# Kernel tuning notes

Hardware: AMD Instinct MI355X
Metric: run time of the kernel (lower is better)

Reference implementation:

```python
import jax, jax.numpy as jnp
import numpy as np

N_NODES = 2048
N_PAIRS = 65536
D = 512
P = 16


def setup_inputs() -> dict:
    key = jax.random.key(0)
    ks = jax.random.split(key, 9)
    scale = 1.0 / np.sqrt(D)
    obj_feats = jax.random.normal(ks[0], (N_NODES, D), dtype=jnp.float32)
    union_feats = jax.random.normal(ks[1], (N_PAIRS, D), dtype=jnp.float32)
    pair_idxs = jax.random.randint(ks[2], (N_PAIRS, 2), 0, N_NODES, dtype=jnp.int64)
    ws_w = jax.random.uniform(ks[3], (D, D), jnp.float32, -scale, scale)
    ws_b = jax.random.uniform(ks[4], (D,), jnp.float32, -scale, scale)
    wo_w = jax.random.uniform(ks[5], (D, D), jnp.float32, -scale, scale)
    wo_b = jax.random.uniform(ks[6], (D,), jnp.float32, -scale, scale)
    w_w = jax.random.uniform(ks[7], (P, D), jnp.float32, -scale, scale)
    w_b = jax.random.uniform(ks[8], (P,), jnp.float32, -scale, scale)
    return {
        'obj_feats': obj_feats, 'union_feats': union_feats, 'pair_idxs': pair_idxs,
        'ws_w': ws_w, 'ws_b': ws_b, 'wo_w': wo_w, 'wo_b': wo_b, 'w_w': w_w, 'w_b': w_b,
    }


def reference(obj_feats, union_feats, pair_idxs, ws_w, ws_b, wo_w, wo_b, w_w, w_b):
    n = obj_feats.shape[0]
    p = w_w.shape[0]
    # node projections: [N, D]
    s = obj_feats @ ws_w.T + ws_b
    o = obj_feats @ wo_w.T + wo_b
    # gather pair features and fuse elementwise product: [E, D]
    prod = s[pair_idxs[:, 0]] * o[pair_idxs[:, 1]] * union_feats
    # project to p attention logits per pair: [E, p]
    atten_f = prod @ w_w.T + w_b
    # scatter into dense [N, N, p]
    atten = jnp.zeros((n, n, p), dtype=obj_feats.dtype)
    atten = atten.at[pair_idxs[:, 0], pair_idxs[:, 1]].add(atten_f)
    # mask diagonal with -1e4 and softmax over axis=1 (incoming nodes)
    atten = atten - jnp.eye(n, dtype=obj_feats.dtype)[:, :, None] * 10000.0
    return jax.nn.softmax(atten, axis=1)
```

## Files before the change

kernel.cpp:

```cpp
#include <hip/hip_runtime.h>
#include <hip/hip_bf16.h>

#define N_NODES 2048
#define N_PAIRS 65536
#define DIM 512
#define NP 16
#define SLOTS 96
#define SP 520

typedef __attribute__((ext_vector_type(8))) short s16x8;
typedef __attribute__((ext_vector_type(8))) unsigned short u16x8;
typedef __attribute__((ext_vector_type(4))) float f32x4;

static __device__ __forceinline__ unsigned short f2bf(float x) {
    union { float f; unsigned int u; } v; v.f = x;
    unsigned int r = v.u + 0x7FFFu + ((v.u >> 16) & 1u);
    return (unsigned short)(r >> 16);
}
static __device__ __forceinline__ float bf2f(unsigned short u) {
    union { unsigned int u; float f; } v; v.u = ((unsigned int)u) << 16;
    return v.f;
}
static __device__ __forceinline__ u16x8 pack8(float4 a, float4 b) {
    u16x8 r;
    r[0]=f2bf(a.x); r[1]=f2bf(a.y); r[2]=f2bf(a.z); r[3]=f2bf(a.w);
    r[4]=f2bf(b.x); r[5]=f2bf(b.y); r[6]=f2bf(b.z); r[7]=f2bf(b.w);
    return r;
}
static __device__ __forceinline__ void store_nt4(float* p, float a, float b, float c, float d) {
    f32x4 v = {a, b, c, d};
    __builtin_nontemporal_store(v, (f32x4*)p);
}

#define GBM 64
#define GBN 64
#define GBK 32
#define GSA 40

__global__ __launch_bounds__(256) void gemm_so(
    const float* __restrict__ A, const float* __restrict__ Ws, const float* __restrict__ bsv,
    const float* __restrict__ Wo, const float* __restrict__ bov,
    unsigned short* __restrict__ Sb, unsigned short* __restrict__ Ob,
    int* __restrict__ rowcnt)
{
    __shared__ unsigned short As[GBM*GSA];
    __shared__ unsigned short Bs[GBN*GSA];
    const int tid = threadIdx.x;
    {
        const int bid = blockIdx.y * gridDim.x + blockIdx.x;
        if (bid < 8) rowcnt[bid*256 + tid] = 0;
    }
    const int m0 = blockIdx.y*GBM, n0 = blockIdx.x*GBN;
    const int ar = tid>>2, ac = (tid&3)*8;
    const float* Arow = A + (size_t)(m0+ar)*DIM + ac;
    const int nrow = n0 + ar;
    const float* Wrow = (nrow < DIM ? Ws + (size_t)nrow*DIM : Wo + (size_t)(nrow-DIM)*DIM) + ac;
    float4 a_r[2], b_r[2];
    a_r[0] = *(const float4*)(Arow);   a_r[1] = *(const float4*)(Arow+4);
    b_r[0] = *(const float4*)(Wrow);   b_r[1] = *(const float4*)(Wrow+4);

    const int lane = tid&63, wid = tid>>6;
    const int wm = (wid>>1)*32, wn = (wid&1)*32;
    const int fr = lane&15, ks8 = (lane>>4)*8;
    f32x4 acc[2][2] = {};
    for (int k0=0; k0<DIM; k0+=GBK) {
        *(u16x8*)&As[ar*GSA+ac] = pack8(a_r[0],a_r[1]);
        *(u16x8*)&Bs[ar*GSA+ac] = pack8(b_r[0],b_r[1]);
        __syncthreads();
        if (k0+GBK < DIM) {
            a_r[0] = *(const float4*)(Arow + k0+GBK);   a_r[1] = *(const float4*)(Arow + k0+GBK + 4);
            b_r[0] = *(const float4*)(Wrow + k0+GBK);   b_r[1] = *(const float4*)(Wrow + k0+GBK + 4);
        }
        s16x8 af[2], bfr[2];
        #pragma unroll
        for (int mi=0;mi<2;++mi) af[mi]  = *(const s16x8*)&As[(wm+mi*16+fr)*GSA + ks8];
        #pragma unroll
        for (int ni=0;ni<2;++ni) bfr[ni] = *(const s16x8*)&Bs[(wn+ni*16+fr)*GSA + ks8];
        #pragma unroll
        for (int mi=0;mi<2;++mi)
            #pragma unroll
            for (int ni=0;ni<2;++ni)
                acc[mi][ni] = __builtin_amdgcn_mfma_f32_16x16x32_bf16(af[mi], bfr[ni], acc[mi][ni], 0,0,0);
        __syncthreads();
    }
    const int rg = lane>>4;
    #pragma unroll
    for (int ni=0;ni<2;++ni) {
        const int n = n0 + wn + ni*16 + fr;
        const float bias = (n < DIM) ? bsv[n] : bov[n-DIM];
        unsigned short* dst = (n < DIM) ? (Sb + n) : (Ob + (n - DIM));
        #pragma unroll
        for (int mi=0;mi<2;++mi) {
            #pragma unroll
            for (int q=0;q<4;++q) {
                const int m = m0 + wm + mi*16 + rg*4 + q;
                dst[(size_t)m*DIM] = f2bf(acc[mi][ni][q] + bias);
            }
        }
    }
}

__global__ __launch_bounds__(256) void pairproj_k(
    const unsigned short* __restrict__ Sb, const unsigned short* __restrict__ Ob,
    const float* __restrict__ U, const int* __restrict__ idx,
    const float* __restrict__ w_w, const float* __restrict__ w_b,
    int* __restrict__ rowcnt, int* __restrict__ rowj, float* __restrict__ rowv)
{
    __shared__ unsigned short P[4*16*SP];
    const int tid = threadIdx.x;
    const int lane = tid&63, wid = tid>>6;
    const int fr = lane&15, ks8 = (lane>>4)*8;
    s16x8 wreg[16];
    #pragma unroll
    for (int st=0;st<16;++st) {
        const float4* wp = (const float4*)(w_w + (size_t)fr*DIM + st*32 + ks8);
        u16x8 t = pack8(wp[0], wp[1]);
        wreg[st] = *(s16x8*)&t;
    }
    const float wbv = w_b[fr];
    unsigned short* Pw = &P[wid*16*SP];
    const int eb = blockIdx.x*128 + wid*32;
    for (int it=0; it<2; ++it) {
        const int e0 = eb + it*16;
        #pragma unroll 4
        for (int s8=0; s8<16; ++s8) {
            const int e = e0 + s8;
            const int i = idx[2*e], j = idx[2*e+1];
            u16x8 sv = *(const u16x8*)(Sb + (size_t)i*DIM + lane*8);
            u16x8 ov = *(const u16x8*)(Ob + (size_t)j*DIM + lane*8);
            const float4* up = (const float4*)(U + (size_t)e*DIM + lane*8);
            float4 u0 = up[0], u1 = up[1];
            float4 p0, p1;
            p0.x = bf2f(sv[0])*bf2f(ov[0])*u0.x;
            p0.y = bf2f(sv[1])*bf2f(ov[1])*u0.y;
            p0.z = bf2f(sv[2])*bf2f(ov[2])*u0.z;
            p0.w = bf2f(sv[3])*bf2f(ov[3])*u0.w;
            p1.x = bf2f(sv[4])*bf2f(ov[4])*u1.x;
            p1.y = bf2f(sv[5])*bf2f(ov[5])*u1.y;
            p1.z = bf2f(sv[6])*bf2f(ov[6])*u1.z;
            p1.w = bf2f(sv[7])*bf2f(ov[7])*u1.w;
            *(u16x8*)&Pw[s8*SP + lane*8] = pack8(p0, p1);
        }
        f32x4 acc = {0.f,0.f,0.f,0.f};
        #pragma unroll
        for (int st=0;st<16;++st) {
            s16x8 af = *(const s16x8*)&Pw[fr*SP + st*32 + ks8];
            acc = __builtin_amdgcn_mfma_f32_16x16x32_bf16(af, wreg[st], acc, 0,0,0);
        }
        int iv = 0, posv = 0;
        if (lane < 16) {
            const int e = e0 + lane;
            iv = idx[2*e];
            const int jv = idx[2*e + 1];
            posv = atomicAdd(&rowcnt[iv], 1);
            if (posv < SLOTS) rowj[iv*SLOTS + posv] = jv;
        }
        const int rg = lane>>4;
        #pragma unroll
        for (int q=0;q<4;++q) {
            const int pr = rg*4 + q;
            const int ip = __shfl(iv, pr, 64);
            const int pp = __shfl(posv, pr, 64);
            if (pp < SLOTS)
                rowv[((size_t)ip*SLOTS + pp)*NP + fr] = acc[q] + wbv;
        }
    }
}

__global__ __launch_bounds__(256) void softmax_k(
    const int* __restrict__ rowcnt, const int* __restrict__ rowj,
    const float* __restrict__ rowv, float* __restrict__ out)
{
    __shared__ __align__(16) float vals[SLOTS][NP];
    __shared__ int jcol[SLOTS];
    __shared__ unsigned char dead[SLOTS];
    __shared__ float red[16][17];
    __shared__ float mP[NP], invZ[NP], bg[NP];
    __shared__ int ndistinct;
    const int i = blockIdx.x;
    const int t = threadIdx.x;
    int c = rowcnt[i];
    if (c > SLOTS) c = SLOTS;

    if (t == 0) ndistinct = 0;
    for (int a = t; a < c; a += 256) {
        jcol[a] = rowj[i*SLOTS + a];
        dead[a] = 0;
        const float4* src = (const float4*)(rowv + ((size_t)i*SLOTS + a)*NP);
        float4* dst = (float4*)vals[a];
        dst[0] = src[0]; dst[1] = src[1]; dst[2] = src[2]; dst[3] = src[3];
    }
    __syncthreads();

    for (int a = t; a < c; a += 256) {
        int j = jcol[a];
        int first = a;
        for (int b = 0; b < a; ++b) if (jcol[b] == j) { first = b; break; }
        if (first != a) {
            dead[a] = 1;
            #pragma unroll
            for (int p = 0; p < NP; ++p) atomicAdd(&vals[first][p], vals[a][p]);
        }
    }
    __syncthreads();
    for (int a = t; a < c; a += 256)
        if (!dead[a] && jcol[a] != i) atomicAdd(&ndistinct, 1);
    __syncthreads();

    const int p = t & 15, ch = t >> 4;
    float pm = 0.f;
    for (int a = ch; a < c; a += 16)
        if (!dead[a] && jcol[a] != i) pm = fmaxf(pm, vals[a][p]);
    red[ch][p] = pm;
    __syncthreads();
    if (t < NP) {
        float m = 0.f;
        #pragma unroll
        for (int k = 0; k < 16; ++k) m = fmaxf(m, red[k][t]);
        mP[t] = m;
    }
    __syncthreads();
    {
        const float m = mP[p];
        float ps = 0.f;
        for (int a = ch; a < c; a += 16)
            if (!dead[a] && jcol[a] != i) ps += __expf(vals[a][p] - m);
        red[ch][p] = ps;
    }
    __syncthreads();
    if (t < NP) {
        float zs = 0.f;
        #pragma unroll
        for (int k = 0; k < 16; ++k) zs += red[k][t];
        const float m = mP[t];
        const float eb = __expf(-m);
        const float nbg = (float)(N_NODES - 1 - ndistinct);
        const float Z = zs + nbg * eb;
        const float iz = 1.0f / Z;
        invZ[t] = iz; bg[t] = eb * iz;
    }
    __syncthreads();

    const size_t rowbase = (size_t)i * N_NODES * NP;
    {
        const int g = t & 3;
        const float b0 = bg[g*4+0], b1 = bg[g*4+1], b2 = bg[g*4+2], b3 = bg[g*4+3];
        float* orow = out + rowbase;
        #pragma unroll 8
        for (int n = 0; n < 32; ++n)
            store_nt4(orow + 4*(t + 256*n), b0, b1, b2, b3);
    }
    __syncthreads();

    for (int a = t; a < c; a += 256) {
        if (dead[a]) continue;
        const int j = jcol[a];
        float* dst = out + rowbase + (size_t)j * NP;
        if (j == i) {
            store_nt4(dst+0,  0.f,0.f,0.f,0.f);
            store_nt4(dst+4,  0.f,0.f,0.f,0.f);
            store_nt4(dst+8,  0.f,0.f,0.f,0.f);
            store_nt4(dst+12, 0.f,0.f,0.f,0.f);
        } else {
            #pragma unroll
            for (int q = 0; q < 4; ++q) {
                store_nt4(dst + 4*q,
                    __expf(vals[a][4*q+0] - mP[4*q+0]) * invZ[4*q+0],
                    __expf(vals[a][4*q+1] - mP[4*q+1]) * invZ[4*q+1],
                    __expf(vals[a][4*q+2] - mP[4*q+2]) * invZ[4*q+2],
                    __expf(vals[a][4*q+3] - mP[4*q+3]) * invZ[4*q+3]);
            }
        }
    }
    if (t == 0) {
        float* dst = out + rowbase + (size_t)i * NP;
        store_nt4(dst+0,  0.f,0.f,0.f,0.f);
        store_nt4(dst+4,  0.f,0.f,0.f,0.f);
        store_nt4(dst+8,  0.f,0.f,0.f,0.f);
        store_nt4(dst+12, 0.f,0.f,0.f,0.f);
    }
}

extern "C" void kernel_launch(void* const* d_in, const int* in_sizes, int n_in,
                              void* d_out, int out_size, void* d_ws, size_t ws_size,
                              hipStream_t stream)
{
    (void)in_sizes; (void)n_in; (void)out_size; (void)ws_size;
    const float* obj  = (const float*)d_in[0];
    const float* uni  = (const float*)d_in[1];
    const int*   idx  = (const int*)  d_in[2];
    const float* ws_w = (const float*)d_in[3];
    const float* ws_b = (const float*)d_in[4];
    const float* wo_w = (const float*)d_in[5];
    const float* wo_b = (const float*)d_in[6];
    const float* w_w  = (const float*)d_in[7];
    const float* w_b  = (const float*)d_in[8];
    float* out = (float*)d_out;

    unsigned short* Sb = (unsigned short*)d_ws;
    unsigned short* Ob = Sb + (size_t)N_NODES * DIM;
    float* rowv  = (float*)(Ob + (size_t)N_NODES * DIM);
    int* rowj    = (int*)(rowv + (size_t)N_NODES * SLOTS * NP);
    int* rowcnt  = rowj + (size_t)N_NODES * SLOTS;

    gemm_so<<<dim3(1024/GBN, N_NODES/GBM), 256, 0, stream>>>(obj, ws_w, ws_b, wo_w, wo_b, Sb, Ob, rowcnt);
    pairproj_k<<<N_PAIRS/128, 256, 0, stream>>>(Sb, Ob, uni, idx, w_w, w_b, rowcnt, rowj, rowv);
    softmax_k<<<N_NODES, 256, 0, stream>>>(rowcnt, rowj, rowv, out);
}
```

Measured before the change: 122.8 us.

## Split pair projection K dimension in halves and shrink per-block pair count

The pair projection kernel now handles 16 pairs per wave instead of 32, so the grid doubles to N_PAIRS/64 blocks. It walks the 512-wide feature dimension in two halves of 256, staging a half-width bf16 tile in shared memory and accumulating MFMA results across the halves. This halves shared memory per block and doubles the number of blocks, aiming for better occupancy and latency hiding on the gather-heavy loads. In exchange, each lane issues narrower 8-byte loads, and the 16 pre-packed weight registers are still loaded once per block, now amortised over half as many pairs.

```diff
diff --git a/kernel.cpp b/kernel.cpp
--- a/kernel.cpp
+++ b/kernel.cpp
@@ -6,10 +6,11 @@
 #define DIM 512
 #define NP 16
 #define SLOTS 96
-#define SP 520
+#define SP2 264
 
 typedef __attribute__((ext_vector_type(8))) short s16x8;
 typedef __attribute__((ext_vector_type(8))) unsigned short u16x8;
+typedef __attribute__((ext_vector_type(4))) unsigned short u16x4;
 typedef __attribute__((ext_vector_type(4))) float f32x4;
 
 static __device__ __forceinline__ unsigned short f2bf(float x) {
@@ -106,7 +107,7 @@
     const float* __restrict__ w_w, const float* __restrict__ w_b,
     int* __restrict__ rowcnt, int* __restrict__ rowj, float* __restrict__ rowv)
 {
-    __shared__ unsigned short P[4*16*SP];
+    __shared__ unsigned short P[4*16*SP2];
     const int tid = threadIdx.x;
     const int lane = tid&63, wid = tid>>6;
     const int fr = lane&15, ks8 = (lane>>4)*8;
@@ -118,52 +119,49 @@
         wreg[st] = *(s16x8*)&t;
     }
     const float wbv = w_b[fr];
-    unsigned short* Pw = &P[wid*16*SP];
-    const int eb = blockIdx.x*128 + wid*32;
-    for (int it=0; it<2; ++it) {
-        const int e0 = eb + it*16;
+    unsigned short* Pw = &P[wid*16*SP2];
+    const int e0 = blockIdx.x*64 + wid*16;
+
+    f32x4 acc = {0.f,0.f,0.f,0.f};
+    #pragma unroll
+    for (int kh=0; kh<2; ++kh) {
+        const int kb = kh*256;
         #pragma unroll 4
         for (int s8=0; s8<16; ++s8) {
             const int e = e0 + s8;
             const int i = idx[2*e], j = idx[2*e+1];
-            u16x8 sv = *(const u16x8*)(Sb + (size_t)i*DIM + lane*8);
-            u16x8 ov = *(const u16x8*)(Ob + (size_t)j*DIM + lane*8);
-            const float4* up = (const float4*)(U + (size_t)e*DIM + lane*8);
-            float4 u0 = up[0], u1 = up[1];
-            float4 p0, p1;
-            p0.x = bf2f(sv[0])*bf2f(ov[0])*u0.x;
-            p0.y = bf2f(sv[1])*bf2f(ov[1])*u0.y;
-            p0.z = bf2f(sv[2])*bf2f(ov[2])*u0.z;
-            p0.w = bf2f(sv[3])*bf2f(ov[3])*u0.w;
-            p1.x = bf2f(sv[4])*bf2f(ov[4])*u1.x;
-            p1.y = bf2f(sv[5])*bf2f(ov[5])*u1.y;
-            p1.z = bf2f(sv[6])*bf2f(ov[6])*u1.z;
-            p1.w = bf2f(sv[7])*bf2f(ov[7])*u1.w;
-            *(u16x8*)&Pw[s8*SP + lane*8] = pack8(p0, p1);
-        }
-        f32x4 acc = {0.f,0.f,0.f,0.f};
-        #pragma unroll
-        for (int st=0;st<16;++st) {
-            s16x8 af = *(const s16x8*)&Pw[fr*SP + st*32 + ks8];
-            acc = __builtin_amdgcn_mfma_f32_16x16x32_bf16(af, wreg[st], acc, 0,0,0);
-        }
-        int iv = 0, posv = 0;
-        if (lane < 16) {
-            const int e = e0 + lane;
-            iv = idx[2*e];
-            const int jv = idx[2*e + 1];
-            posv = atomicAdd(&rowcnt[iv], 1);
-            if (posv < SLOTS) rowj[iv*SLOTS + posv] = jv;
-        }
-        const int rg = lane>>4;
-        #pragma unroll
-        for (int q=0;q<4;++q) {
-            const int pr = rg*4 + q;
-            const int ip = __shfl(iv, pr, 64);
-            const int pp = __shfl(posv, pr, 64);
-            if (pp < SLOTS)
-                rowv[((size_t)ip*SLOTS + pp)*NP + fr] = acc[q] + wbv;
-        }
+            u16x4 sv = *(const u16x4*)(Sb + (size_t)i*DIM + kb + lane*4);
+            u16x4 ov = *(const u16x4*)(Ob + (size_t)j*DIM + kb + lane*4);
+            float4 uv = *(const float4*)(U + (size_t)e*DIM + kb + lane*4);
+            u16x4 pk;
+            pk[0] = f2bf(bf2f(sv[0])*bf2f(ov[0])*uv.x);
+            pk[1] = f2bf(bf2f(sv[1])*bf2f(ov[1])*uv.y);
+            pk[2] = f2bf(bf2f(sv[2])*bf2f(ov[2])*uv.z);
+            pk[3] = f2bf(bf2f(sv[3])*bf2f(ov[3])*uv.w);
+            *(u16x4*)&Pw[s8*SP2 + lane*4] = pk;
+        }
+        #pragma unroll
+        for (int st=0;st<8;++st) {
+            s16x8 af = *(const s16x8*)&Pw[fr*SP2 + st*32 + ks8];
+            acc = __builtin_amdgcn_mfma_f32_16x16x32_bf16(af, wreg[kh*8+st], acc, 0,0,0);
+        }
+    }
+    int iv = 0, posv = 0;
+    if (lane < 16) {
+        const int e = e0 + lane;
+        iv = idx[2*e];
+        const int jv = idx[2*e + 1];
+        posv = atomicAdd(&rowcnt[iv], 1);
+        if (posv < SLOTS) rowj[iv*SLOTS + posv] = jv;
+    }
+    const int rg = lane>>4;
+    #pragma unroll
+    for (int q=0;q<4;++q) {
+        const int pr = rg*4 + q;
+        const int ip = __shfl(iv, pr, 64);
+        const int pp = __shfl(posv, pr, 64);
+        if (pp < SLOTS)
+            rowv[((size_t)ip*SLOTS + pp)*NP + fr] = acc[q] + wbv;
     }
 }
 
@@ -304,6 +302,6 @@
     int* rowcnt  = rowj + (size_t)N_NODES * SLOTS;
 
     gemm_so<<<dim3(1024/GBN, N_NODES/GBM), 256, 0, stream>>>(obj, ws_w, ws_b, wo_w, wo_b, Sb, Ob, rowcnt);
-    pairproj_k<<<N_PAIRS/128, 256, 0, stream>>>(Sb, Ob, uni, idx, w_w, w_b, rowcnt, rowj, rowv);
+    pairproj_k<<<N_PAIRS/64, 256, 0, stream>>>(Sb, Ob, uni, idx, w_w, w_b, rowcnt, rowj, rowv);
     softmax_k<<<N_NODES, 256, 0, stream>>>(rowcnt, rowj, rowv, out);
 }
```

Measured after the change: 128.5 us. +4.6%, slower.
